# Kernel tuning notes

Measured on AMD Instinct MI355X. Metric: run time of the kernel, lower is better.

Reference implementation:

```python
import jax, jax.numpy as jnp
import numpy as np

L1, L2, N, C = 4096, 4096, 8, 3


def setup_inputs() -> dict:
    key = jax.random.key(0)
    k1, k2 = jax.random.split(key)
    coords1 = jax.random.uniform(k1, (L1, N, C), dtype=jnp.float32)
    coords2 = jax.random.uniform(k2, (L2, N, C), dtype=jnp.float32)
    return {"coords1": coords1, "coords2": coords2}


def reference(coords1, coords2):
    # coords1: [L1, N, C], coords2: [L2, N, C]
    l1, n, c = coords1.shape
    l2 = coords2.shape[0]
    # Batch-first layout, matching flatten_batch semantics (per-batch NN only)
    q = jnp.swapaxes(coords2, 0, 1)  # [N, L2, C] query points
    r = jnp.swapaxes(coords1, 0, 1)  # [N, L1, C] reference points
    # Squared euclidean distances per batch: [N, L2, L1]
    d2 = (
        jnp.sum(q * q, axis=-1)[:, :, None]
        + jnp.sum(r * r, axis=-1)[:, None, :]
        - 2.0 * jnp.einsum("nlc,nmc->nlm", q, r)
    )
    # tc.nearest returns global flat index; original does fmod(L1) to get the
    # per-batch index — argmin within each batch gives that directly.
    nearest = jnp.argmin(d2, axis=-1)  # [N, L2]
    clusters = nearest.T  # [L2, N]
    # torch.meshgrid(arange(L2), arange(N)) with 'ij' indexing; indices[-1] is
    # the batch index broadcast to [L2, N].
    batch_idx = jnp.broadcast_to(jnp.arange(n, dtype=jnp.int64 if False else jnp.int32), (l2, n))
    return (clusters.reshape(-1), batch_idx.reshape(-1))
```

## Files before the change

kernel.cpp:

```cpp
#include <hip/hip_runtime.h>
#include <float.h>
#include <limits.h>


constexpr int kL1 = 4096, kL2 = 4096, kN = 8;
constexpr int kCS = 520;
constexpr size_t kOffPts = 8ull * kCS * 4;
constexpr size_t kWsBytes = kOffPts + 8ull * kL1 * 16;

__device__ __forceinline__ float rr_exact(float x, float y, float z) {
  return __fadd_rn(__fadd_rn(__fmul_rn(x, x), __fmul_rn(y, y)), __fmul_rn(z, z));
}

__global__ __launch_bounds__(1024)
void bin_kernel(const float* __restrict__ c1, int* __restrict__ cellStart,
                float4* __restrict__ pts) {
#pragma clang fp contract(off)
  __shared__ int cnt[512];
  const int tid = threadIdx.x;
  const int n = blockIdx.x;
  if (tid < 512) cnt[tid] = 0;
  __syncthreads();

  float xs[4], ys[4], zs[4];
  int cl[4];
#pragma unroll
  for (int k = 0; k < 4; ++k) {
    const int j = k * 1024 + tid;
    const float* p = c1 + (j * kN + n) * 3;
    const float x = p[0], y = p[1], z = p[2];
    xs[k] = x; ys[k] = y; zs[k] = z;
    const int cx = min(7, max(0, (int)(x * 8.0f)));
    const int cy = min(7, max(0, (int)(y * 8.0f)));
    const int cz = min(7, max(0, (int)(z * 8.0f)));
    cl[k] = (cz * 8 + cy) * 8 + cx;
    atomicAdd(&cnt[cl[k]], 1);
  }
  __syncthreads();

  if (tid < 64) {
    int loc[8], part = 0;
#pragma unroll
    for (int i = 0; i < 8; ++i) { loc[i] = cnt[tid * 8 + i]; part += loc[i]; }
    int inc = part;
#pragma unroll
    for (int off = 1; off < 64; off <<= 1) {
      const int v = __shfl_up(inc, off);
      if (tid >= off) inc += v;
    }
    int base = inc - part;
#pragma unroll
    for (int i = 0; i < 8; ++i) {
      const int c = tid * 8 + i;
      cellStart[n * kCS + c] = base;
      cnt[c] = base;
      base += loc[i];
    }
    if (tid == 0) cellStart[n * kCS + 512] = kL1;
  }
  __syncthreads();

#pragma unroll
  for (int k = 0; k < 4; ++k) {
    const int j = k * 1024 + tid;
    const int pos = atomicAdd(&cnt[cl[k]], 1);
    pts[n * kL1 + pos] = make_float4(xs[k], ys[k], zs[k], __int_as_float(j));
  }
}

__global__ __launch_bounds__(256, 6)
void grid_nn_kernel(const int* __restrict__ cellStart, const float4* __restrict__ pts,
                    const float* __restrict__ c2, int* __restrict__ out) {
#pragma clang fp contract(off)
  const int n = blockIdx.y;
  const int wave = threadIdx.x >> 6;
  const int lane = threadIdx.x & 63;
  const int qj = blockIdx.x * 4 + wave;

  const float* p = c2 + (qj * kN + n) * 3;
  const float qx = p[0], qy = p[1], qz = p[2];
  const float qq = rr_exact(qx, qy, qz);
  const int cx = min(7, max(0, (int)(qx * 8.0f)));
  const int cy = min(7, max(0, (int)(qy * 8.0f)));
  const int cz = min(7, max(0, (int)(qz * 8.0f)));
  const int xlo = max(0, cx - 1), xhi = min(7, cx + 1);

  const int* __restrict__ cs = cellStart + n * kCS;
  const float4* __restrict__ P = pts + n * kL1;

  int S[9], Lk[9], pre[10];
#pragma unroll
  for (int k = 0; k < 9; ++k) {
    const int dz = k / 3 - 1, dy = k % 3 - 1;
    const int z = cz + dz, y = cy + dy;
    const bool valid = ((unsigned)z <= 7u) && ((unsigned)y <= 7u);
    const int zc = min(7, max(0, z)), yc = min(7, max(0, y));
    const int row = (zc * 8 + yc) * 8;
    const int s = cs[row + xlo];
    const int e = cs[row + xhi + 1];
    S[k] = s;
    Lk[k] = valid ? (e - s) : 0;
  }
  pre[0] = 0;
#pragma unroll
  for (int k = 0; k < 9; ++k) pre[k + 1] = pre[k] + Lk[k];
  const int T = pre[9];

  float bd = FLT_MAX;
  int bi = INT_MAX;

  for (int base = 0; base < T; base += 256) {
    int g[4], a[4];
#pragma unroll
    for (int u = 0; u < 4; ++u) {
      g[u] = base + lane + u * 64;
      int ad = 0;
#pragma unroll
      for (int k = 0; k < 9; ++k) {
        const bool in = (g[u] >= pre[k]) && (g[u] < pre[k + 1]);
        ad = in ? (S[k] + (g[u] - pre[k])) : ad;
      }
      a[u] = ad;
    }
    float4 rp[4];
#pragma unroll
    for (int u = 0; u < 4; ++u) rp[u] = P[a[u]];
#pragma unroll
    for (int u = 0; u < 4; ++u) {
      const int id = __float_as_int(rp[u].w);
      const float rr = rr_exact(rp[u].x, rp[u].y, rp[u].z);
      const float dot = __fadd_rn(
          __fadd_rn(__fmul_rn(qx, rp[u].x), __fmul_rn(qy, rp[u].y)),
          __fmul_rn(qz, rp[u].z));
      const float d2 = __fmaf_rn(-2.0f, dot, __fadd_rn(qq, rr));
      if (g[u] < T && (d2 < bd || (d2 == bd && id < bi))) { bd = d2; bi = id; }
    }
  }

#pragma unroll
  for (int m = 1; m <= 32; m <<= 1) {
    const float od = __shfl_xor(bd, m);
    const int oi = __shfl_xor(bi, m);
    if (od < bd || (od == bd && oi < bi)) { bd = od; bi = oi; }
  }

  if (!(0.015625f > __fadd_rn(bd, 4e-6f))) {
    for (int pp = lane; pp < kL1; pp += 64) {
      const float4 rp = P[pp];
      const int id = __float_as_int(rp.w);
      const float rr = rr_exact(rp.x, rp.y, rp.z);
      const float dot = __fadd_rn(
          __fadd_rn(__fmul_rn(qx, rp.x), __fmul_rn(qy, rp.y)),
          __fmul_rn(qz, rp.z));
      const float d2 = __fmaf_rn(-2.0f, dot, __fadd_rn(qq, rr));
      if (d2 < bd || (d2 == bd && id < bi)) { bd = d2; bi = id; }
    }
#pragma unroll
    for (int m = 1; m <= 32; m <<= 1) {
      const float od = __shfl_xor(bd, m);
      const int oi = __shfl_xor(bi, m);
      if (od < bd || (od == bd && oi < bi)) { bd = od; bi = oi; }
    }
  }

  if (lane == 0) {
    out[qj * kN + n] = bi;
    out[kL2 * kN + qj * kN + n] = n;
  }
}

constexpr int kQPerBlock = 16;
constexpr int kQ = 4;
constexpr int kChunk = 1024;

__global__ __launch_bounds__(256, 4)
void nearest_kernel_lds(const float* __restrict__ c1, const float* __restrict__ c2,
                        int* __restrict__ out) {
#pragma clang fp contract(off)
  __shared__ float sRx[kChunk], sRy[kChunk], sRz[kChunk], sRr[kChunk];
  const int tid = threadIdx.x;
  const int n = blockIdx.y;
  const int wave = tid >> 6;
  const int lane = tid & 63;
  const int q0 = blockIdx.x * kQPerBlock + wave * kQ;

  float qxs[kQ], qys[kQ], qzs[kQ], qqs[kQ];
#pragma unroll
  for (int i = 0; i < kQ; ++i) {
    const float* p = c2 + ((q0 + i) * kN + n) * 3;
    qxs[i] = p[0]; qys[i] = p[1]; qzs[i] = p[2];
    qqs[i] = rr_exact(qxs[i], qys[i], qzs[i]);
  }
  float bd[kQ]; int bt[kQ];
#pragma unroll
  for (int i = 0; i < kQ; ++i) { bd[i] = FLT_MAX; bt[i] = 0; }

  for (int chunk = 0; chunk < kL1 / kChunk; ++chunk) {
    __syncthreads();
    {
      const int jb = chunk * kChunk + tid * 4;
      float x[4], y[4], z[4], w4[4];
#pragma unroll
      for (int k = 0; k < 4; ++k) {
        const float* p = c1 + ((jb + k) * kN + n) * 3;
        x[k] = p[0]; y[k] = p[1]; z[k] = p[2];
        w4[k] = rr_exact(x[k], y[k], z[k]);
      }
      *reinterpret_cast<float4*>(&sRx[tid * 4]) = make_float4(x[0], x[1], x[2], x[3]);
      *reinterpret_cast<float4*>(&sRy[tid * 4]) = make_float4(y[0], y[1], y[2], y[3]);
      *reinterpret_cast<float4*>(&sRz[tid * 4]) = make_float4(z[0], z[1], z[2], z[3]);
      *reinterpret_cast<float4*>(&sRr[tid * 4]) = make_float4(w4[0], w4[1], w4[2], w4[3]);
    }
    __syncthreads();
#pragma unroll
    for (int t = 0; t < kChunk / 256; ++t) {
      const int tg = chunk * (kChunk / 256) + t;
      const int base = t * 256 + lane * 4;
      const float4 x4 = *reinterpret_cast<const float4*>(&sRx[base]);
      const float4 y4 = *reinterpret_cast<const float4*>(&sRy[base]);
      const float4 z4 = *reinterpret_cast<const float4*>(&sRz[base]);
      const float4 r4 = *reinterpret_cast<const float4*>(&sRr[base]);
      const float xs[4] = {x4.x, x4.y, x4.z, x4.w};
      const float ys[4] = {y4.x, y4.y, y4.z, y4.w};
      const float zs[4] = {z4.x, z4.y, z4.z, z4.w};
      const float rs[4] = {r4.x, r4.y, r4.z, r4.w};
#pragma unroll
      for (int i = 0; i < kQ; ++i) {
        float d[4];
#pragma unroll
        for (int k = 0; k < 4; ++k) {
          const float dot = __fadd_rn(
              __fadd_rn(__fmul_rn(qxs[i], xs[k]), __fmul_rn(qys[i], ys[k])),
              __fmul_rn(qzs[i], zs[k]));
          d[k] = __fmaf_rn(-2.0f, dot, __fadd_rn(qqs[i], rs[k]));
        }
        const float old = bd[i];
        float m = fminf(fminf(d[0], d[1]), old);
        m = fminf(fminf(d[2], d[3]), m);
        bd[i] = m;
        if (m < old) bt[i] = tg;
      }
    }
  }
  int sel[kQ];
#pragma unroll
  for (int i = 0; i < kQ; ++i) sel[i] = bt[i] * 64 + lane;
#pragma unroll
  for (int m = 1; m <= 32; m <<= 1) {
#pragma unroll
    for (int i = 0; i < kQ; ++i) {
      const float od = __shfl_xor(bd[i], m);
      const int os = __shfl_xor(sel[i], m);
      if (od < bd[i] || (od == bd[i] && os < sel[i])) { bd[i] = od; sel[i] = os; }
    }
  }
#pragma unroll
  for (int i = 0; i < kQ; ++i) {
    if (lane == i) {
      const int j0 = sel[i] * 4;
      float best = FLT_MAX; int kk = 0;
#pragma unroll
      for (int k = 0; k < 4; ++k) {
        const float* p = c1 + ((j0 + k) * kN + n) * 3;
        const float r0 = p[0], r1 = p[1], r2 = p[2];
        const float rr = rr_exact(r0, r1, r2);
        const float dot = __fadd_rn(
            __fadd_rn(__fmul_rn(qxs[i], r0), __fmul_rn(qys[i], r1)),
            __fmul_rn(qzs[i], r2));
        const float dc = __fmaf_rn(-2.0f, dot, __fadd_rn(qqs[i], rr));
        if (dc < best) { best = dc; kk = k; }
      }
      out[(q0 + i) * kN + n] = j0 + kk;
      out[kL2 * kN + (q0 + i) * kN + n] = n;
    }
  }
}

extern "C" void kernel_launch(void* const* d_in, const int* in_sizes, int n_in,
                              void* d_out, int out_size, void* d_ws, size_t ws_size,
                              hipStream_t stream) {
  const float* c1 = (const float*)d_in[0];
  const float* c2 = (const float*)d_in[1];
  int* out = (int*)d_out;
  if (d_ws != nullptr && ws_size >= kWsBytes) {
    int* cellStart = (int*)d_ws;
    float4* pts = (float4*)((char*)d_ws + kOffPts);
    bin_kernel<<<dim3(kN), dim3(1024), 0, stream>>>(c1, cellStart, pts);
    grid_nn_kernel<<<dim3(kL2 / 4, kN), dim3(256), 0, stream>>>(
        cellStart, pts, c2, out);
  } else {
    dim3 grid(kL2 / kQPerBlock, kN);
    nearest_kernel_lds<<<grid, dim3(256), 0, stream>>>(c1, c2, out);
  }
}
```

Baseline: 82.18 us.

## Split binning into cell-index, histogram-scan, and global-atomic scatter kernels

The single 8-block binning kernel is replaced by three kernels. A wide kernel computes each point's cell index, a small kernel builds the per-batch histogram and prefix scan and writes cursors, and a wide kernel scatters points into cell order using global atomics. The goal is to spread the coordinate loads and scatter across many blocks instead of only 8, at the cost of two extra launches, extra global traffic and global atomic contention. Point order within a cell now depends on atomic timing, which can change tie-breaking in the nearest-neighbour search.

```diff
diff --git a/kernel.cpp b/kernel.cpp
--- a/kernel.cpp
+++ b/kernel.cpp
@@ -5,43 +5,49 @@
 
 constexpr int kL1 = 4096, kL2 = 4096, kN = 8;
 constexpr int kCS = 520;
-constexpr size_t kOffPts = 8ull * kCS * 4;
+constexpr size_t kOffCursor = 8ull * kCS * 4;
+constexpr size_t kOffCellOf = kOffCursor + 8ull * 512 * 4;
+constexpr size_t kOffPts = kOffCellOf + 32768ull * 4;
 constexpr size_t kWsBytes = kOffPts + 8ull * kL1 * 16;
 
 __device__ __forceinline__ float rr_exact(float x, float y, float z) {
   return __fadd_rn(__fadd_rn(__fmul_rn(x, x), __fmul_rn(y, y)), __fmul_rn(z, z));
 }
 
+__device__ __forceinline__ int cell_of(float x, float y, float z) {
+  const int cx = min(7, max(0, (int)(x * 8.0f)));
+  const int cy = min(7, max(0, (int)(y * 8.0f)));
+  const int cz = min(7, max(0, (int)(z * 8.0f)));
+  return (cz * 8 + cy) * 8 + cx;
+}
+
+__global__ __launch_bounds__(256)
+void cellof_kernel(const float* __restrict__ c1, int* __restrict__ cellOf) {
+  const int t = blockIdx.x * 256 + threadIdx.x;
+  const float x = c1[3 * t], y = c1[3 * t + 1], z = c1[3 * t + 2];
+  cellOf[t] = cell_of(x, y, z);
+}
+
 __global__ __launch_bounds__(1024)
-void bin_kernel(const float* __restrict__ c1, int* __restrict__ cellStart,
-                float4* __restrict__ pts) {
-#pragma clang fp contract(off)
-  __shared__ int cnt[512];
+void histscan_kernel(const int* __restrict__ cellOf, int* __restrict__ cellStart,
+                     int* __restrict__ cursor) {
+  __shared__ int hist[512];
   const int tid = threadIdx.x;
   const int n = blockIdx.x;
-  if (tid < 512) cnt[tid] = 0;
+  if (tid < 512) hist[tid] = 0;
   __syncthreads();
 
-  float xs[4], ys[4], zs[4];
-  int cl[4];
 #pragma unroll
   for (int k = 0; k < 4; ++k) {
     const int j = k * 1024 + tid;
-    const float* p = c1 + (j * kN + n) * 3;
-    const float x = p[0], y = p[1], z = p[2];
-    xs[k] = x; ys[k] = y; zs[k] = z;
-    const int cx = min(7, max(0, (int)(x * 8.0f)));
-    const int cy = min(7, max(0, (int)(y * 8.0f)));
-    const int cz = min(7, max(0, (int)(z * 8.0f)));
-    cl[k] = (cz * 8 + cy) * 8 + cx;
-    atomicAdd(&cnt[cl[k]], 1);
+    atomicAdd(&hist[cellOf[j * kN + n]], 1);
   }
   __syncthreads();
 
   if (tid < 64) {
     int loc[8], part = 0;
 #pragma unroll
-    for (int i = 0; i < 8; ++i) { loc[i] = cnt[tid * 8 + i]; part += loc[i]; }
+    for (int i = 0; i < 8; ++i) { loc[i] = hist[tid * 8 + i]; part += loc[i]; }
     int inc = part;
 #pragma unroll
     for (int off = 1; off < 64; off <<= 1) {
@@ -53,19 +59,23 @@
     for (int i = 0; i < 8; ++i) {
       const int c = tid * 8 + i;
       cellStart[n * kCS + c] = base;
-      cnt[c] = base;
+      cursor[n * 512 + c] = base;
       base += loc[i];
     }
     if (tid == 0) cellStart[n * kCS + 512] = kL1;
   }
-  __syncthreads();
-
-#pragma unroll
-  for (int k = 0; k < 4; ++k) {
-    const int j = k * 1024 + tid;
-    const int pos = atomicAdd(&cnt[cl[k]], 1);
-    pts[n * kL1 + pos] = make_float4(xs[k], ys[k], zs[k], __int_as_float(j));
-  }
+}
+
+__global__ __launch_bounds__(256)
+void scatter_kernel(const float* __restrict__ c1, const int* __restrict__ cellOf,
+                    int* __restrict__ cursor, float4* __restrict__ pts) {
+  const int t = blockIdx.x * 256 + threadIdx.x;
+  const int n = t & (kN - 1);
+  const int j = t >> 3;
+  const float x = c1[3 * t], y = c1[3 * t + 1], z = c1[3 * t + 2];
+  const int cell = cellOf[t];
+  const int pos = atomicAdd(&cursor[n * 512 + cell], 1);
+  pts[n * kL1 + pos] = make_float4(x, y, z, __int_as_float(j));
 }
 
 __global__ __launch_bounds__(256, 6)
@@ -284,8 +294,13 @@
   int* out = (int*)d_out;
   if (d_ws != nullptr && ws_size >= kWsBytes) {
     int* cellStart = (int*)d_ws;
+    int* cursor = (int*)((char*)d_ws + kOffCursor);
+    int* cellOf = (int*)((char*)d_ws + kOffCellOf);
     float4* pts = (float4*)((char*)d_ws + kOffPts);
-    bin_kernel<<<dim3(kN), dim3(1024), 0, stream>>>(c1, cellStart, pts);
+    cellof_kernel<<<dim3(kL1 * kN / 256), dim3(256), 0, stream>>>(c1, cellOf);
+    histscan_kernel<<<dim3(kN), dim3(1024), 0, stream>>>(cellOf, cellStart, cursor);
+    scatter_kernel<<<dim3(kL1 * kN / 256), dim3(256), 0, stream>>>(
+        c1, cellOf, cursor, pts);
     grid_nn_kernel<<<dim3(kL2 / 4, kN), dim3(256), 0, stream>>>(
         cellStart, pts, c2, out);
   } else {
```

New measurement: 84.47 us. 2.8% more time.

## Materialize per-cell contiguous neighbor point lists for grid nearest-neighbor search

Applied to the files above, without the earlier changes.

Adds an expand kernel that copies, for every grid cell, the points of its 3x3 row neighborhood into one contiguous padded list with indices stored separately. The query kernel then reads these lists with contiguous vector loads and no per-element segment lookup over nine ranges. Squared norms are also precomputed into the w component during binning. In exchange it adds an extra kernel launch, a much larger workspace, and a copy pass of roughly 100k points per batch. It also relies on the workspace being large enough, otherwise the fallback path runs.

```diff
diff --git a/kernel.cpp b/kernel.cpp
--- a/kernel.cpp
+++ b/kernel.cpp
@@ -5,8 +5,14 @@
 
 constexpr int kL1 = 4096, kL2 = 4096, kN = 8;
 constexpr int kCS = 520;
-constexpr size_t kOffPts = 8ull * kCS * 4;
-constexpr size_t kWsBytes = kOffPts + 8ull * kL1 * 16;
+constexpr int kNbrCap = 112640;
+constexpr size_t kOffNbrStart = 8ull * kCS * 4;
+constexpr size_t kOffNbrLen = kOffNbrStart + 8ull * kCS * 4;
+constexpr size_t kOffPidx = kOffNbrLen + 8ull * 512 * 4;
+constexpr size_t kOffPts4 = kOffPidx + 8ull * kL1 * 4;
+constexpr size_t kOffNbrIdx = kOffPts4 + 8ull * kL1 * 16;
+constexpr size_t kOffNbrPts = kOffNbrIdx + 8ull * kNbrCap * 4;
+constexpr size_t kWsBytes = kOffNbrPts + 8ull * kNbrCap * 16;
 
 __device__ __forceinline__ float rr_exact(float x, float y, float z) {
   return __fadd_rn(__fadd_rn(__fmul_rn(x, x), __fmul_rn(y, y)), __fmul_rn(z, z));
@@ -14,9 +20,11 @@
 
 __global__ __launch_bounds__(1024)
 void bin_kernel(const float* __restrict__ c1, int* __restrict__ cellStart,
-                float4* __restrict__ pts) {
+                int* __restrict__ nbrStart, int* __restrict__ nbrLen,
+                float4* __restrict__ pts4, int* __restrict__ pidx) {
 #pragma clang fp contract(off)
   __shared__ int cnt[512];
+  __shared__ int st[513];
   const int tid = threadIdx.x;
   const int n = blockIdx.x;
   if (tid < 512) cnt[tid] = 0;
@@ -53,10 +61,11 @@
     for (int i = 0; i < 8; ++i) {
       const int c = tid * 8 + i;
       cellStart[n * kCS + c] = base;
+      st[c] = base;
       cnt[c] = base;
       base += loc[i];
     }
-    if (tid == 0) cellStart[n * kCS + 512] = kL1;
+    if (tid == 0) { cellStart[n * kCS + 512] = kL1; st[512] = kL1; }
   }
   __syncthreads();
 
@@ -64,12 +73,93 @@
   for (int k = 0; k < 4; ++k) {
     const int j = k * 1024 + tid;
     const int pos = atomicAdd(&cnt[cl[k]], 1);
-    pts[n * kL1 + pos] = make_float4(xs[k], ys[k], zs[k], __int_as_float(j));
+    pts4[n * kL1 + pos] =
+        make_float4(xs[k], ys[k], zs[k], rr_exact(xs[k], ys[k], zs[k]));
+    pidx[n * kL1 + pos] = j;
+  }
+  __syncthreads();
+
+  int Tc = 0;
+  if (tid < 512) {
+    const int cx = tid & 7, cy = (tid >> 3) & 7, cz = tid >> 6;
+    const int xlo = max(0, cx - 1), xhi = min(7, cx + 1);
+#pragma unroll
+    for (int k = 0; k < 9; ++k) {
+      const int dz = k / 3 - 1, dy = k % 3 - 1;
+      const int z = cz + dz, y = cy + dy;
+      if (((unsigned)z <= 7u) && ((unsigned)y <= 7u)) {
+        const int row = (z * 8 + y) * 8;
+        Tc += st[row + xhi + 1] - st[row + xlo];
+      }
+    }
+  }
+  __syncthreads();
+  if (tid < 512) cnt[tid] = Tc;
+  __syncthreads();
+
+  if (tid < 64) {
+    int loc[8], pad[8], part = 0;
+#pragma unroll
+    for (int i = 0; i < 8; ++i) {
+      loc[i] = cnt[tid * 8 + i];
+      pad[i] = (loc[i] + 3) & ~3;
+      part += pad[i];
+    }
+    int inc = part;
+#pragma unroll
+    for (int off = 1; off < 64; off <<= 1) {
+      const int v = __shfl_up(inc, off);
+      if (tid >= off) inc += v;
+    }
+    int base = inc - part;
+#pragma unroll
+    for (int i = 0; i < 8; ++i) {
+      const int c = tid * 8 + i;
+      nbrStart[n * kCS + c] = base;
+      nbrLen[n * 512 + c] = loc[i];
+      base += pad[i];
+    }
+  }
+}
+
+__global__ __launch_bounds__(256)
+void expand_kernel(const int* __restrict__ cellStart, const int* __restrict__ nbrStart,
+                   const float4* __restrict__ pts4, const int* __restrict__ pidx,
+                   float4* __restrict__ nbrPts, int* __restrict__ nbrIdx) {
+  const int wg = blockIdx.x * 4 + (threadIdx.x >> 6);
+  const int lane = threadIdx.x & 63;
+  const int n = wg & 7, cell = wg >> 3;
+  const int cx = cell & 7, cy = (cell >> 3) & 7, cz = cell >> 6;
+  const int xlo = max(0, cx - 1), xhi = min(7, cx + 1);
+  const int* __restrict__ cs = cellStart + n * kCS;
+  const float4* __restrict__ P = pts4 + n * kL1;
+  const int* __restrict__ I = pidx + n * kL1;
+  const int d0 = nbrStart[n * kCS + cell];
+  float4* __restrict__ DP = nbrPts + (size_t)n * kNbrCap + d0;
+  int* __restrict__ DI = nbrIdx + (size_t)n * kNbrCap + d0;
+
+  int dst = 0;
+#pragma unroll
+  for (int k = 0; k < 9; ++k) {
+    const int dz = k / 3 - 1, dy = k % 3 - 1;
+    const int z = cz + dz, y = cy + dy;
+    if (((unsigned)z <= 7u) && ((unsigned)y <= 7u)) {
+      const int row = (z * 8 + y) * 8;
+      const int s = cs[row + xlo];
+      const int len = cs[row + xhi + 1] - s;
+      for (int i = lane; i < len; i += 64) {
+        DP[dst + i] = P[s + i];
+        DI[dst + i] = I[s + i];
+      }
+      dst += len;
+    }
   }
 }
 
 __global__ __launch_bounds__(256, 6)
-void grid_nn_kernel(const int* __restrict__ cellStart, const float4* __restrict__ pts,
+void grid_nn_kernel(const int* __restrict__ nbrStart, const int* __restrict__ nbrLen,
+                    const float4* __restrict__ nbrPts, const int* __restrict__ nbrIdx,
+                    const float4* __restrict__ pts4, const int* __restrict__ pidx,
                     const float* __restrict__ c2, int* __restrict__ out) {
 #pragma clang fp contract(off)
   const int n = blockIdx.y;
@@ -83,57 +173,32 @@
   const int cx = min(7, max(0, (int)(qx * 8.0f)));
   const int cy = min(7, max(0, (int)(qy * 8.0f)));
   const int cz = min(7, max(0, (int)(qz * 8.0f)));
-  const int xlo = max(0, cx - 1), xhi = min(7, cx + 1);
-
-  const int* __restrict__ cs = cellStart + n * kCS;
-  const float4* __restrict__ P = pts + n * kL1;
-
-  int S[9], Lk[9], pre[10];
-#pragma unroll
-  for (int k = 0; k < 9; ++k) {
-    const int dz = k / 3 - 1, dy = k % 3 - 1;
-    const int z = cz + dz, y = cy + dy;
-    const bool valid = ((unsigned)z <= 7u) && ((unsigned)y <= 7u);
-    const int zc = min(7, max(0, z)), yc = min(7, max(0, y));
-    const int row = (zc * 8 + yc) * 8;
-    const int s = cs[row + xlo];
-    const int e = cs[row + xhi + 1];
-    S[k] = s;
-    Lk[k] = valid ? (e - s) : 0;
-  }
-  pre[0] = 0;
-#pragma unroll
-  for (int k = 0; k < 9; ++k) pre[k + 1] = pre[k] + Lk[k];
-  const int T = pre[9];
+  const int cell = (cz * 8 + cy) * 8 + cx;
+
+  const int start = nbrStart[n * kCS + cell];
+  const int T = nbrLen[n * 512 + cell];
+  const float4* __restrict__ CP = nbrPts + (size_t)n * kNbrCap + start;
+  const int* __restrict__ CI = nbrIdx + (size_t)n * kNbrCap + start;
 
   float bd = FLT_MAX;
   int bi = INT_MAX;
 
   for (int base = 0; base < T; base += 256) {
-    int g[4], a[4];
+    const int s0 = base + lane * 4;
+    const int4 id4 = *reinterpret_cast<const int4*>(CI + s0);
+    const int idv[4] = {id4.x, id4.y, id4.z, id4.w};
+    float4 rp[4];
+#pragma unroll
+    for (int u = 0; u < 4; ++u) rp[u] = CP[s0 + u];
 #pragma unroll
     for (int u = 0; u < 4; ++u) {
-      g[u] = base + lane + u * 64;
-      int ad = 0;
-#pragma unroll
-      for (int k = 0; k < 9; ++k) {
-        const bool in = (g[u] >= pre[k]) && (g[u] < pre[k + 1]);
-        ad = in ? (S[k] + (g[u] - pre[k])) : ad;
-      }
-      a[u] = ad;
-    }
-    float4 rp[4];
-#pragma unroll
-    for (int u = 0; u < 4; ++u) rp[u] = P[a[u]];
-#pragma unroll
-    for (int u = 0; u < 4; ++u) {
-      const int id = __float_as_int(rp[u].w);
-      const float rr = rr_exact(rp[u].x, rp[u].y, rp[u].z);
       const float dot = __fadd_rn(
           __fadd_rn(__fmul_rn(qx, rp[u].x), __fmul_rn(qy, rp[u].y)),
           __fmul_rn(qz, rp[u].z));
-      const float d2 = __fmaf_rn(-2.0f, dot, __fadd_rn(qq, rr));
-      if (g[u] < T && (d2 < bd || (d2 == bd && id < bi))) { bd = d2; bi = id; }
+      const float d2 = __fmaf_rn(-2.0f, dot, __fadd_rn(qq, rp[u].w));
+      if (s0 + u < T && (d2 < bd || (d2 == bd && idv[u] < bi))) {
+        bd = d2; bi = idv[u];
+      }
     }
   }
 
@@ -145,14 +210,15 @@
   }
 
   if (!(0.015625f > __fadd_rn(bd, 4e-6f))) {
+    const float4* __restrict__ P = pts4 + n * kL1;
+    const int* __restrict__ I = pidx + n * kL1;
     for (int pp = lane; pp < kL1; pp += 64) {
       const float4 rp = P[pp];
-      const int id = __float_as_int(rp.w);
-      const float rr = rr_exact(rp.x, rp.y, rp.z);
+      const int id = I[pp];
       const float dot = __fadd_rn(
           __fadd_rn(__fmul_rn(qx, rp.x), __fmul_rn(qy, rp.y)),
           __fmul_rn(qz, rp.z));
-      const float d2 = __fmaf_rn(-2.0f, dot, __fadd_rn(qq, rr));
+      const float d2 = __fmaf_rn(-2.0f, dot, __fadd_rn(qq, rp.w));
       if (d2 < bd || (d2 == bd && id < bi)) { bd = d2; bi = id; }
     }
 #pragma unroll
@@ -284,10 +350,18 @@
   int* out = (int*)d_out;
   if (d_ws != nullptr && ws_size >= kWsBytes) {
     int* cellStart = (int*)d_ws;
-    float4* pts = (float4*)((char*)d_ws + kOffPts);
-    bin_kernel<<<dim3(kN), dim3(1024), 0, stream>>>(c1, cellStart, pts);
+    int* nbrStart = (int*)((char*)d_ws + kOffNbrStart);
+    int* nbrLen = (int*)((char*)d_ws + kOffNbrLen);
+    int* pidx = (int*)((char*)d_ws + kOffPidx);
+    float4* pts4 = (float4*)((char*)d_ws + kOffPts4);
+    int* nbrIdx = (int*)((char*)d_ws + kOffNbrIdx);
+    float4* nbrPts = (float4*)((char*)d_ws + kOffNbrPts);
+    bin_kernel<<<dim3(kN), dim3(1024), 0, stream>>>(c1, cellStart, nbrStart,
+                                                    nbrLen, pts4, pidx);
+    expand_kernel<<<dim3(1024), dim3(256), 0, stream>>>(cellStart, nbrStart,
+                                                        pts4, pidx, nbrPts, nbrIdx);
     grid_nn_kernel<<<dim3(kL2 / 4, kN), dim3(256), 0, stream>>>(
-        cellStart, pts, c2, out);
+        nbrStart, nbrLen, nbrPts, nbrIdx, pts4, pidx, c2, out);
   } else {
     dim3 grid(kL2 / kQPerBlock, kN);
     nearest_kernel_lds<<<grid, dim3(256), 0, stream>>>(c1, c2, out);
```

New measurement: 91.90 us. 11.8% more time.
